# Kernel optimization log

Hardware: AMD Instinct MI355X
Metric: run time of the kernel (lower is better)

## Reference

```python
import jax, jax.numpy as jnp
import numpy as np

EPS = 1e-8
NUM_LAYERS = 6


def setup_inputs() -> dict:
    key = jax.random.key(0)
    ks = jax.random.split(key, 8)
    N, Cin, Cout, S, H, W = 4, 256, 256, 512, 64, 64
    fan_in = Cin  # kaiming for 1x1 conv, leaky_relu a=0 -> gain sqrt(2)
    return {
        "x": jax.random.normal(ks[0], (N, Cin, H, W), dtype=jnp.float32),
        "y": jax.random.normal(ks[1], (N, S), dtype=jnp.float32),
        "ch_conv_w": jax.random.normal(ks[2], (Cout, Cin), dtype=jnp.float32) / np.sqrt(fan_in),
        "ch_conv_b": jnp.zeros((Cout,), dtype=jnp.float32),
        "affine_w": jax.random.normal(ks[3], (NUM_LAYERS, Cout, S), dtype=jnp.float32) / np.sqrt(S),
        "affine_b": jnp.zeros((NUM_LAYERS, Cout), dtype=jnp.float32),
        "mod_w": jax.random.normal(ks[4], (NUM_LAYERS, Cout, Cout), dtype=jnp.float32) * np.sqrt(2.0 / Cout),
    }


def _forward(x, y, ch_conv_w, ch_conv_b, affine_w, affine_b, mod_w):
    # 1x1 channel conv (with bias)
    x = jnp.einsum("oi,bihw->bohw", ch_conv_w, x) + ch_conv_b[None, :, None, None]
    x = jnp.repeat(jnp.repeat(x, 2, axis=2), 2, axis=3)
    # channel repeat_interleave(2) -> [N, 2C, H, W]
    x = jnp.repeat(x, 2, axis=1)

    C = x.shape[1] // 2
    for i in range(NUM_LAYERS):
        x1, x2 = x[:, :C], x[:, C:]
        # SpatialShift2d with default directions pads [1,1,1,1] (replicate) then
        # crops the identical region for every split -> exact identity.
        y1 = x1 + x2
        # g-branch: Conv2dMod(k=1) with per-sample style modulation + exact GELU
        s = jnp.einsum("cs,bs->bc", affine_w[i], y) + affine_b[i]  # [B, C]
        wmod = mod_w[i][None] * (s[:, :, None] + 1.0)              # [B, O, I] (style scales OUTPUT channel)
        d = jax.lax.rsqrt(jnp.sum(wmod * wmod, axis=2, keepdims=True) + EPS)
        wmod = wmod * d
        h = jnp.einsum("boi,bihw->bohw", wmod, y1)
        y2 = x2 + jax.nn.gelu(h, approximate=False)
        x = jnp.concatenate([y1, y2], axis=1)

    x1, x2 = x[:, :C], x[:, C:]
    return (x1 + x2) * 0.5


def reference(x, y, ch_conv_w, ch_conv_b, affine_w, affine_b, mod_w):
    return _forward(x, y, ch_conv_w, ch_conv_b, affine_w, affine_b, mod_w)
```

## Files before the change

### kernel.cpp

```cpp
#include <hip/hip_runtime.h>
#include <math.h>

#define NB 4
#define CC 256
#define SS 512
#define NL 6
#define SLOT_HW 65536
#define G_OFF_HW   (7*SLOT_HW)

typedef __attribute__((ext_vector_type(8))) short s16x8;
typedef __attribute__((ext_vector_type(4))) float f32x4;
typedef __attribute__((ext_vector_type(2))) float f32x2;
typedef __attribute__((ext_vector_type(4))) unsigned short u16x4;

__device__ __forceinline__ unsigned short f2bf(float f) {
    unsigned u = __builtin_bit_cast(unsigned, f);
    u += 0x7FFFu + ((u >> 16) & 1u);
    return (unsigned short)(u >> 16);
}
__device__ __forceinline__ unsigned cvt_pk_bf16(float lo, float hi) {
    unsigned r;
    asm("v_cvt_pk_bf16_f32 %0, %1, %2" : "=v"(r) : "v"(lo), "v"(hi));
    return r;
}
__device__ __forceinline__ float gelu_fast(float x) {
    float u = x * (1.0f + 0.044715f * x * x);
    float e = __expf(-1.5957691216f * u);
    return x * __builtin_amdgcn_rcpf(1.0f + e);
}


__global__ __launch_bounds__(256) void prep_kernel(
    const float* __restrict__ y, const float* __restrict__ aw,
    const float* __restrict__ ab, const float* __restrict__ mw,
    const float* __restrict__ cw, unsigned short* __restrict__ wsBF)
{
    int w = threadIdx.x >> 6, lane = threadIdx.x & 63;
    float* gtab = (float*)(wsBF + G_OFF_HW);

    if (blockIdx.x < 448) {
        int row = blockIdx.x*4 + w;
        int sl  = row >> 8, m = row & 255;
        const float* src = (sl == 0) ? (cw + (size_t)m*CC)
                                     : (mw + ((size_t)(sl-1)*CC + m)*CC);
        unsigned short* dst = wsBF + (size_t)sl*SLOT_HW;
#pragma unroll
        for (int u = 0; u < 4; ++u) {
            int k = lane + 64*u;
            int f = (m >> 4)*8 + (k >> 5);
            int hw = f*512 + ((k >> 3) & 3)*128 + (m & 15)*8 + (k & 7);
            dst[hw] = f2bf(src[k]);
        }
        return;
    }

    int r  = (blockIdx.x - 448)*4 + w;
    int pl = r >> 8, po = r & 255;

    const float* awr = aw + (size_t)(pl*CC + po)*SS;
    float s[4] = {0.f, 0.f, 0.f, 0.f};
#pragma unroll
    for (int j = 0; j < 8; ++j) {
        int idx = lane + 64*j;
        float a = awr[idx];
#pragma unroll
        for (int b = 0; b < 4; ++b) s[b] += a * y[(size_t)b*SS + idx];
    }
    const float* mwr = mw + ((size_t)pl*CC + po)*CC;
    float qs = 0.f;
#pragma unroll
    for (int u = 0; u < 4; ++u) { float v = mwr[lane + 64*u]; qs += v*v; }
#pragma unroll
    for (int off = 32; off; off >>= 1) {
#pragma unroll
        for (int b = 0; b < 4; ++b) s[b] += __shfl_xor(s[b], off);
        qs += __shfl_xor(qs, off);
    }
    float abv = ab[pl*CC + po];
    if (lane < 4) {
        float t = s[lane] + abv + 1.0f;
        gtab[pl*1024 + lane*256 + po] = t * (1.0f / sqrtf(t*t*qs + 1e-8f));
    }
}

#define BFRAGL(buf, kq, nt, kcl) \
    (lds + (buf)*16384 + ((((kq)*2 + (nt))*2 + (kcl)))*1024)

__global__ __launch_bounds__(512, 4) void fused_kernel(
    const float* __restrict__ x, const float* __restrict__ cb,
    const unsigned short* __restrict__ wsBF, float* __restrict__ out)
{
    __shared__ __align__(16) unsigned char lds[69632];
    float* xS = (float*)(lds + 32768);
    float* S2 = (float*)(lds + 32768);
    const float* gtab = (const float*)(wsBF + G_OFF_HW);

    const int tid  = threadIdx.x;
    const int lane = tid & 63;
    const int w    = tid >> 6;
    const int l15  = lane & 15;
    const int q    = lane >> 4;

    const int bswz  = blockIdx.x & 7;
    const int b     = bswz >> 1;
    const int half  = bswz & 1;
    const int strip = blockIdx.x >> 3;
    const int n0    = strip * 64 + half * 32;

    float y1[2][2][4], y2[2][2][4];
    f32x4 acc[2][2];

#pragma unroll
    for (int t = 0; t < 2; ++t)
#pragma unroll
        for (int s = 0; s < 2; ++s) acc[t][s] = 0;

    float4 xr[4];
#pragma unroll
    for (int p = 0; p < 4; ++p) {
        int row = (tid >> 3) + 64*p, c4 = (tid & 7) * 4;
        xr[p] = *(const float4*)&x[((size_t)(b*CC + row))*4096 + n0 + c4];
    }
    s16x8 aS[8][2];
#pragma unroll
    for (int p = 0; p < 4; ++p)
#pragma unroll
    for (int t = 0; t < 2; ++t)
        aS[p][t] = *(const s16x8*)(wsBF + (size_t)(((2*w+t)*8 + p)*512) + lane*8);

#pragma unroll
    for (int p = 0; p < 4; ++p) {
        int row = (tid >> 3) + 64*p, c4 = (tid & 7) * 4;
        *(float4*)&xS[row*36 + c4] = xr[p];
    }
    __syncthreads();
    {
        int n = tid & 31, k0 = (tid >> 5) * 16;
        int nt = n >> 4, n15 = n & 15;
#pragma unroll
        for (int j = 0; j < 4; ++j) {
            int k = k0 + 4*j;
            float v0 = xS[(k+0)*36 + n], v1 = xS[(k+1)*36 + n];
            float v2 = xS[(k+2)*36 + n], v3 = xS[(k+3)*36 + n];
            uint2 hv; hv.x = cvt_pk_bf16(v0, v1); hv.y = cvt_pk_bf16(v2, v3);
            int kq = k >> 6, kcl = (k >> 5) & 1, qq = (k >> 3) & 3, jb = k & 7;
            *(uint2*)(BFRAGL(0,kq,nt,kcl) + (16*qq + n15)*16 + jb*2) = hv;
        }
    }
    __syncthreads();
    {
        const unsigned short* slot = wsBF;
        __builtin_amdgcn_s_setprio(1);
#pragma unroll
        for (int step = 0; step < 8; ++step) {
            if (step < 4) {
#pragma unroll
                for (int t = 0; t < 2; ++t)
                    aS[step+4][t] = *(const s16x8*)(slot + (size_t)(((2*w+t)*8 + step+4)*512) + lane*8);
            }
            int kq = step >> 1, kcl = step & 1;
#pragma unroll
            for (int s = 0; s < 2; ++s) {
                s16x8 bh = *(const s16x8*)(BFRAGL(0,kq,s,kcl) + lane*16);
#pragma unroll
                for (int t = 0; t < 2; ++t)
                    acc[t][s] = __builtin_amdgcn_mfma_f32_16x16x32_bf16(aS[step][t], bh, acc[t][s], 0, 0, 0);
            }
        }
        __builtin_amdgcn_s_setprio(0);
    }

#pragma unroll
    for (int pass = 0; pass < 2; ++pass) {
        __syncthreads();
        if ((w >> 2) == pass) {
#pragma unroll
            for (int t = 0; t < 2; ++t)
#pragma unroll
            for (int s = 0; s < 2; ++s)
#pragma unroll
            for (int r = 0; r < 4; ++r) {
                int m  = 32*w + 16*t + 4*q + r;
                int nl = 16*s + l15;
                S2[(m - 128*pass)*33 + nl] = acc[t][s][r] + cb[m];
            }
        }
        __syncthreads();
#pragma unroll
        for (int t = 0; t < 2; ++t)
#pragma unroll
        for (int s = 0; s < 2; ++s)
#pragma unroll
        for (int r = 0; r < 4; ++r) {
            int c  = 32*w + 16*t + 4*q + r;
            int nl = 16*s + l15;
            float v = S2[(c >> 1)*33 + nl];
            if (pass == 0) { y1[t][s][r] = v; }
            else           { y2[t][s][r] = v; y1[t][s][r] += v; }
        }
    }

    for (int l = 0; l < NL; ++l) {
        const int buf = l & 1;
        const unsigned short* slot = wsBF + (size_t)(1 + l)*SLOT_HW;
#pragma unroll
        for (int t = 0; t < 2; ++t)
#pragma unroll
            for (int s = 0; s < 2; ++s) acc[t][s] = 0;

#pragma unroll
        for (int p = 0; p < 4; ++p)
#pragma unroll
        for (int t = 0; t < 2; ++t)
            aS[p][t] = *(const s16x8*)(slot + (size_t)(((2*w+t)*8 + p)*512) + lane*8);
        float4 gv[2];
#pragma unroll
        for (int t = 0; t < 2; ++t)
            gv[t] = *(const float4*)&gtab[l*1024 + b*256 + 32*w + 16*t + 4*q];

        {
            int kq = w >> 1, kcl = w & 1, jb = 4*(q & 1);
#pragma unroll
            for (int t = 0; t < 2; ++t) {
                int qq = 2*t + (q >> 1);
#pragma unroll
                for (int s = 0; s < 2; ++s) {
                    uint2 hv;
                    hv.x = cvt_pk_bf16(y1[t][s][0], y1[t][s][1]);
                    hv.y = cvt_pk_bf16(y1[t][s][2], y1[t][s][3]);
                    *(uint2*)(BFRAGL(buf,kq,s,kcl) + (16*qq + l15)*16 + jb*2) = hv;
                }
            }
        }
        __syncthreads();
        __builtin_amdgcn_s_setprio(1);
#pragma unroll
        for (int step = 0; step < 8; ++step) {
            if (step < 4) {
#pragma unroll
                for (int t = 0; t < 2; ++t)
                    aS[step+4][t] = *(const s16x8*)(slot + (size_t)(((2*w+t)*8 + step+4)*512) + lane*8);
            }
            int kq = step >> 1, kcl = step & 1;
#pragma unroll
            for (int s = 0; s < 2; ++s) {
                s16x8 bh = *(const s16x8*)(BFRAGL(buf,kq,s,kcl) + lane*16);
#pragma unroll
                for (int t = 0; t < 2; ++t)
                    acc[t][s] = __builtin_amdgcn_mfma_f32_16x16x32_bf16(aS[step][t], bh, acc[t][s], 0, 0, 0);
            }
        }
        __builtin_amdgcn_s_setprio(0);
#pragma unroll
        for (int t = 0; t < 2; ++t)
#pragma unroll
        for (int s = 0; s < 2; ++s)
#pragma unroll
        for (int r = 0; r < 4; ++r) {
            y2[t][s][r] += gelu_fast(acc[t][s][r] * gv[t][r]);
            if (l < NL - 1) y1[t][s][r] += y2[t][s][r];
        }
    }

#pragma unroll
    for (int t = 0; t < 2; ++t)
#pragma unroll
    for (int s = 0; s < 2; ++s)
#pragma unroll
    for (int r = 0; r < 4; ++r) {
        int ch  = 32*w + 16*t + 4*q + r;
        int wpx = half*32 + 16*s + l15;
        float v = 0.5f*(y1[t][s][r] + y2[t][s][r]);
        f32x2 vv = {v, v};
        size_t base = (((size_t)(b*CC + ch)*128 + 2*strip))*128 + 2*wpx;
        __builtin_nontemporal_store(vv, (f32x2*)&out[base]);
        __builtin_nontemporal_store(vv, (f32x2*)&out[base + 128]);
    }
}

extern "C" void kernel_launch(void* const* d_in, const int* in_sizes, int n_in,
                              void* d_out, int out_size, void* d_ws, size_t ws_size,
                              hipStream_t stream) {
    const float* x  = (const float*)d_in[0];
    const float* y  = (const float*)d_in[1];
    const float* cw = (const float*)d_in[2];
    const float* cb = (const float*)d_in[3];
    const float* aw = (const float*)d_in[4];
    const float* ab = (const float*)d_in[5];
    const float* mw = (const float*)d_in[6];
    float* out = (float*)d_out;

    unsigned short* wsBF = (unsigned short*)d_ws;

    prep_kernel<<<832, 256, 0, stream>>>(y, aw, ab, mw, cw, wsBF);
    fused_kernel<<<512, 512, 0, stream>>>(x, cb, wsBF, out);
}
```

Baseline: 119.7 us.

## Merge pixel halves into 64-pixel tiles with 1024-thread blocks

```diff
diff --git a/kernel.cpp b/kernel.cpp
--- a/kernel.cpp
+++ b/kernel.cpp
@@ -11,7 +11,6 @@
 typedef __attribute__((ext_vector_type(8))) short s16x8;
 typedef __attribute__((ext_vector_type(4))) float f32x4;
 typedef __attribute__((ext_vector_type(2))) float f32x2;
-typedef __attribute__((ext_vector_type(4))) unsigned short u16x4;
 
 __device__ __forceinline__ unsigned short f2bf(float f) {
     unsigned u = __builtin_bit_cast(unsigned, f);
@@ -83,29 +82,29 @@
     }
 }
 
-#define BFRAGL(buf, kq, nt, kcl) \
-    (lds + (buf)*16384 + ((((kq)*2 + (nt))*2 + (kcl)))*1024)
-
-__global__ __launch_bounds__(512, 4) void fused_kernel(
+#define BFRAG64(buf, kq, nt, kcl) \
+    (lds + (buf)*32768 + ((((kq)*4 + (nt))*2 + (kcl)))*1024)
+
+__global__ __launch_bounds__(1024, 4) void fused_kernel(
     const float* __restrict__ x, const float* __restrict__ cb,
     const unsigned short* __restrict__ wsBF, float* __restrict__ out)
 {
-    __shared__ __align__(16) unsigned char lds[69632];
-    float* xS = (float*)(lds + 32768);
-    float* S2 = (float*)(lds + 32768);
+    __shared__ __align__(16) unsigned char lds[135168];
+    float* xS = (float*)(lds + 65536);
+    float* S2 = (float*)(lds + 65536);
     const float* gtab = (const float*)(wsBF + G_OFF_HW);
 
     const int tid  = threadIdx.x;
     const int lane = tid & 63;
     const int w    = tid >> 6;
+    const int wm   = w & 7;
+    const int wn   = w >> 3;
     const int l15  = lane & 15;
     const int q    = lane >> 4;
 
-    const int bswz  = blockIdx.x & 7;
-    const int b     = bswz >> 1;
-    const int half  = bswz & 1;
-    const int strip = blockIdx.x >> 3;
-    const int n0    = strip * 64 + half * 32;
+    const int b     = blockIdx.x & 3;
+    const int strip = blockIdx.x >> 2;
+    const int n0    = strip * 64;
 
     float y1[2][2][4], y2[2][2][4];
     f32x4 acc[2][2];
@@ -118,7 +117,7 @@
     float4 xr[4];
 #pragma unroll
     for (int p = 0; p < 4; ++p) {
-        int row = (tid >> 3) + 64*p, c4 = (tid & 7) * 4;
+        int row = (tid >> 4) + 64*p, c4 = (tid & 15) * 4;
         xr[p] = *(const float4*)&x[((size_t)(b*CC + row))*4096 + n0 + c4];
     }
     s16x8 aS[8][2];
@@ -126,25 +125,25 @@
     for (int p = 0; p < 4; ++p)
 #pragma unroll
     for (int t = 0; t < 2; ++t)
-        aS[p][t] = *(const s16x8*)(wsBF + (size_t)(((2*w+t)*8 + p)*512) + lane*8);
+        aS[p][t] = *(const s16x8*)(wsBF + (size_t)(((2*wm+t)*8 + p)*512) + lane*8);
 
 #pragma unroll
     for (int p = 0; p < 4; ++p) {
-        int row = (tid >> 3) + 64*p, c4 = (tid & 7) * 4;
-        *(float4*)&xS[row*36 + c4] = xr[p];
+        int row = (tid >> 4) + 64*p, c4 = (tid & 15) * 4;
+        *(float4*)&xS[row*68 + c4] = xr[p];
     }
     __syncthreads();
     {
-        int n = tid & 31, k0 = (tid >> 5) * 16;
+        int n = tid & 63, k0 = (tid >> 6) * 16;
         int nt = n >> 4, n15 = n & 15;
 #pragma unroll
         for (int j = 0; j < 4; ++j) {
             int k = k0 + 4*j;
-            float v0 = xS[(k+0)*36 + n], v1 = xS[(k+1)*36 + n];
-            float v2 = xS[(k+2)*36 + n], v3 = xS[(k+3)*36 + n];
+            float v0 = xS[(k+0)*68 + n], v1 = xS[(k+1)*68 + n];
+            float v2 = xS[(k+2)*68 + n], v3 = xS[(k+3)*68 + n];
             uint2 hv; hv.x = cvt_pk_bf16(v0, v1); hv.y = cvt_pk_bf16(v2, v3);
             int kq = k >> 6, kcl = (k >> 5) & 1, qq = (k >> 3) & 3, jb = k & 7;
-            *(uint2*)(BFRAGL(0,kq,nt,kcl) + (16*qq + n15)*16 + jb*2) = hv;
+            *(uint2*)(BFRAG64(0,kq,nt,kcl) + (16*qq + n15)*16 + jb*2) = hv;
         }
     }
     __syncthreads();
@@ -156,12 +155,12 @@
             if (step < 4) {
 #pragma unroll
                 for (int t = 0; t < 2; ++t)
-                    aS[step+4][t] = *(const s16x8*)(slot + (size_t)(((2*w+t)*8 + step+4)*512) + lane*8);
+                    aS[step+4][t] = *(const s16x8*)(slot + (size_t)(((2*wm+t)*8 + step+4)*512) + lane*8);
             }
             int kq = step >> 1, kcl = step & 1;
 #pragma unroll
             for (int s = 0; s < 2; ++s) {
-                s16x8 bh = *(const s16x8*)(BFRAGL(0,kq,s,kcl) + lane*16);
+                s16x8 bh = *(const s16x8*)(BFRAG64(0,kq,wn*2+s,kcl) + lane*16);
 #pragma unroll
                 for (int t = 0; t < 2; ++t)
                     acc[t][s] = __builtin_amdgcn_mfma_f32_16x16x32_bf16(aS[step][t], bh, acc[t][s], 0, 0, 0);
@@ -173,16 +172,16 @@
 #pragma unroll
     for (int pass = 0; pass < 2; ++pass) {
         __syncthreads();
-        if ((w >> 2) == pass) {
+        if ((wm >> 2) == pass) {
 #pragma unroll
             for (int t = 0; t < 2; ++t)
 #pragma unroll
             for (int s = 0; s < 2; ++s)
 #pragma unroll
             for (int r = 0; r < 4; ++r) {
-                int m  = 32*w + 16*t + 4*q + r;
-                int nl = 16*s + l15;
-                S2[(m - 128*pass)*33 + nl] = acc[t][s][r] + cb[m];
+                int m  = 32*wm + 16*t + 4*q + r;
+                int nl = wn*32 + 16*s + l15;
+                S2[(m - 128*pass)*65 + nl] = acc[t][s][r] + cb[m];
             }
         }
         __syncthreads();
@@ -192,9 +191,9 @@
         for (int s = 0; s < 2; ++s)
 #pragma unroll
         for (int r = 0; r < 4; ++r) {
-            int c  = 32*w + 16*t + 4*q + r;
-            int nl = 16*s + l15;
-            float v = S2[(c >> 1)*33 + nl];
+            int c  = 32*wm + 16*t + 4*q + r;
+            int nl = wn*32 + 16*s + l15;
+            float v = S2[(c >> 1)*65 + nl];
             if (pass == 0) { y1[t][s][r] = v; }
             else           { y2[t][s][r] = v; y1[t][s][r] += v; }
         }
@@ -212,14 +211,14 @@
         for (int p = 0; p < 4; ++p)
 #pragma unroll
         for (int t = 0; t < 2; ++t)
-            aS[p][t] = *(const s16x8*)(slot + (size_t)(((2*w+t)*8 + p)*512) + lane*8);
+            aS[p][t] = *(const s16x8*)(slot + (size_t)(((2*wm+t)*8 + p)*512) + lane*8);
         float4 gv[2];
 #pragma unroll
         for (int t = 0; t < 2; ++t)
-            gv[t] = *(const float4*)&gtab[l*1024 + b*256 + 32*w + 16*t + 4*q];
+            gv[t] = *(const float4*)&gtab[l*1024 + b*256 + 32*wm + 16*t + 4*q];
 
         {
-            int kq = w >> 1, kcl = w & 1, jb = 4*(q & 1);
+            int kq = wm >> 1, kcl = wm & 1, jb = 4*(q & 1);
 #pragma unroll
             for (int t = 0; t < 2; ++t) {
                 int qq = 2*t + (q >> 1);
@@ -228,7 +227,7 @@
                     uint2 hv;
                     hv.x = cvt_pk_bf16(y1[t][s][0], y1[t][s][1]);
                     hv.y = cvt_pk_bf16(y1[t][s][2], y1[t][s][3]);
-                    *(uint2*)(BFRAGL(buf,kq,s,kcl) + (16*qq + l15)*16 + jb*2) = hv;
+                    *(uint2*)(BFRAG64(buf,kq,wn*2+s,kcl) + (16*qq + l15)*16 + jb*2) = hv;
                 }
             }
         }
@@ -239,12 +238,12 @@
             if (step < 4) {
 #pragma unroll
                 for (int t = 0; t < 2; ++t)
-                    aS[step+4][t] = *(const s16x8*)(slot + (size_t)(((2*w+t)*8 + step+4)*512) + lane*8);
+                    aS[step+4][t] = *(const s16x8*)(slot + (size_t)(((2*wm+t)*8 + step+4)*512) + lane*8);
             }
             int kq = step >> 1, kcl = step & 1;
 #pragma unroll
             for (int s = 0; s < 2; ++s) {
-                s16x8 bh = *(const s16x8*)(BFRAGL(buf,kq,s,kcl) + lane*16);
+                s16x8 bh = *(const s16x8*)(BFRAG64(buf,kq,wn*2+s,kcl) + lane*16);
 #pragma unroll
                 for (int t = 0; t < 2; ++t)
                     acc[t][s] = __builtin_amdgcn_mfma_f32_16x16x32_bf16(aS[step][t], bh, acc[t][s], 0, 0, 0);
@@ -268,8 +267,8 @@
     for (int s = 0; s < 2; ++s)
 #pragma unroll
     for (int r = 0; r < 4; ++r) {
-        int ch  = 32*w + 16*t + 4*q + r;
-        int wpx = half*32 + 16*s + l15;
+        int ch  = 32*wm + 16*t + 4*q + r;
+        int wpx = wn*32 + 16*s + l15;
         float v = 0.5f*(y1[t][s][r] + y2[t][s][r]);
         f32x2 vv = {v, v};
         size_t base = (((size_t)(b*CC + ch)*128 + 2*strip))*128 + 2*wpx;
@@ -293,5 +292,5 @@
     unsigned short* wsBF = (unsigned short*)d_ws;
 
     prep_kernel<<<832, 256, 0, stream>>>(y, aw, ab, mw, cw, wsBF);
-    fused_kernel<<<512, 512, 0, stream>>>(x, cb, wsBF, out);
-}
+    fused_kernel<<<256, 1024, 0, stream>>>(x, cb, wsBF, out);
+}
```

After: 120.9 us. About the same (+1.0%).
